# Performance work log

Measured on AMD Instinct MI355X. Metric: run time of the kernel, lower is better.

The kernel has to match this reference:

```python
import jax, jax.numpy as jnp
import numpy as np

HEAD_SIZE = 8
QK_DIM = 512
V_DIM = 512
N = 4096
ATT_DIM = QK_DIM // HEAD_SIZE  # 64
SCALE = ATT_DIM ** (-0.5)
NEG_FILL = jnp.float32(-9e15)


def setup_inputs() -> dict:
    key = jax.random.key(0)
    k1, k2, k3, k4 = jax.random.split(key, 4)
    x1 = jax.random.normal(k1, (N, QK_DIM), dtype=jnp.float32)
    x2 = jax.random.normal(k2, (N, QK_DIM), dtype=jnp.float32)
    v = jax.random.normal(k3, (N, V_DIM), dtype=jnp.float32)
    adj = jax.random.randint(k4, (N, N), 0, 2, dtype=jnp.int32)
    return {"x1": x1, "x2": x2, "v": v, "adj": adj}


def reference(x1, x2, v, adj):
    n = x1.shape[0]
    # [N, H, d] -> [H, N, d]
    q = x1.reshape(n, HEAD_SIZE, -1).transpose(1, 0, 2) * SCALE
    k = x2.reshape(n, HEAD_SIZE, -1).transpose(1, 0, 2)
    vv = v.reshape(n, HEAD_SIZE, -1).transpose(1, 0, 2)
    # [H, N, N] dense scores, masked by adjacency (broadcast over heads)
    scores = jnp.einsum('hnd,hmd->hnm', q, k)
    scores = jnp.where(adj > 0, scores, NEG_FILL)
    attn = jax.nn.softmax(scores, axis=-1)
    out = jnp.einsum('hnm,hmd->hnd', attn, vv)
    # [H, N, d] -> [N, H*d]
    return out.transpose(1, 0, 2).reshape(n, -1)
```

## Files before the change

### kernel.cpp

```cpp
#include <hip/hip_runtime.h>

#define NN 4096
#define HEADS 8
#define DD 64
#define QKD 512

typedef __attribute__((ext_vector_type(8))) short short8;
typedef __attribute__((ext_vector_type(4))) float f32x4;
typedef __attribute__((ext_vector_type(4))) float float4v;
typedef __attribute__((ext_vector_type(4))) int int4v;
typedef unsigned int u32;
typedef unsigned short u16;
typedef unsigned long long u64;

union U8 { u16 u[8]; short8 s; };
union U4 { u32 u[4]; short8 s; };

__device__ __forceinline__ u16 f2bf(float f) {
  u32 u = __float_as_uint(f);
  u += 0x7fffu + ((u >> 16) & 1u);
  return (u16)(u >> 16);
}

__device__ __forceinline__ u32 cvtpk(float lo, float hi) {
  u32 d;
  asm("v_cvt_pk_bf16_f32 %0, %1, %2" : "=v"(d) : "v"(lo), "v"(hi));
  return d;
}

#define GLL(src, dst) __builtin_amdgcn_global_load_lds( \
    (const __attribute__((address_space(1))) void*)(src), \
    (__attribute__((address_space(3))) void*)(dst), 16, 0, 0)

__global__ __launch_bounds__(256) void prepass_fused(
    const float* __restrict__ x2, const float* __restrict__ v,
    const int* __restrict__ adj,
    u16* __restrict__ Kbt, u16* __restrict__ Vbt, u64* __restrict__ Abg)
{
  __shared__ u16 Vtmp[64][80];
  const int b = blockIdx.x;
  const int t = threadIdx.x;

  if (b < 4096) {
    const int row = b;
    const int* src = adj + (size_t)row * NN;
    int4v a0 = *(const int4v*)(src + t * 16);
    int4v a1 = *(const int4v*)(src + t * 16 + 4);
    int4v a2 = *(const int4v*)(src + t * 16 + 8);
    int4v a3 = *(const int4v*)(src + t * 16 + 12);
    u32 bits =
        (u32)(a0.x > 0)         | ((u32)(a0.y > 0) << 1)  |
        ((u32)(a0.z > 0) << 2)  | ((u32)(a0.w > 0) << 3)  |
        ((u32)(a1.x > 0) << 4)  | ((u32)(a1.y > 0) << 5)  |
        ((u32)(a1.z > 0) << 6)  | ((u32)(a1.w > 0) << 7)  |
        ((u32)(a2.x > 0) << 8)  | ((u32)(a2.y > 0) << 9)  |
        ((u32)(a2.z > 0) << 10) | ((u32)(a2.w > 0) << 11) |
        ((u32)(a3.x > 0) << 12) | ((u32)(a3.y > 0) << 13) |
        ((u32)(a3.z > 0) << 14) | ((u32)(a3.w > 0) << 15);
    unsigned char* AB = (unsigned char*)Vtmp;
    *(u16*)(AB + t * 2) = (u16)bits;
    __syncthreads();
    if (t < 64) {
      u64 m = *(const u64*)(AB + t * 8);
      Abg[(size_t)row * 64 + t] = m;
    }
  } else if (b < 4608) {
    const int j = b - 4096;
    const int h = j >> 6, kb = j & 63;
    u16* dst = Kbt + (size_t)j * 4096;
    #pragma unroll
    for (int i = 0; i < 2; i++) {
      int c = t + i * 256;
      int off = c * 16;
      int kr = off >> 7;
      int db = (off & 127) ^ ((kr & 7) << 4);
      int d0 = db >> 1;
      const float* p = x2 + (size_t)(kb * 64 + kr) * QKD + h * DD + d0;
      float4v a0 = *(const float4v*)p;
      float4v a1 = *(const float4v*)(p + 4);
      U8 r;
      r.u[0] = f2bf(a0.x); r.u[1] = f2bf(a0.y); r.u[2] = f2bf(a0.z); r.u[3] = f2bf(a0.w);
      r.u[4] = f2bf(a1.x); r.u[5] = f2bf(a1.y); r.u[6] = f2bf(a1.z); r.u[7] = f2bf(a1.w);
      *(short8*)((char*)dst + off) = r.s;
    }
  } else {
    const int bb = b - 4608;
    const int h = bb >> 6, kb = bb & 63;
    {
      int k = t >> 2, j0 = (t & 3) * 16;
      const float* p = v + (size_t)(kb * 64 + k) * QKD + h * DD + j0;
      float4v a0 = *(const float4v*)p;
      float4v a1 = *(const float4v*)(p + 4);
      float4v a2 = *(const float4v*)(p + 8);
      float4v a3 = *(const float4v*)(p + 12);
      U8 r0, r1;
      r0.u[0] = f2bf(a0.x); r0.u[1] = f2bf(a0.y); r0.u[2] = f2bf(a0.z); r0.u[3] = f2bf(a0.w);
      r0.u[4] = f2bf(a1.x); r0.u[5] = f2bf(a1.y); r0.u[6] = f2bf(a1.z); r0.u[7] = f2bf(a1.w);
      r1.u[0] = f2bf(a2.x); r1.u[1] = f2bf(a2.y); r1.u[2] = f2bf(a2.z); r1.u[3] = f2bf(a2.w);
      r1.u[4] = f2bf(a3.x); r1.u[5] = f2bf(a3.y); r1.u[6] = f2bf(a3.z); r1.u[7] = f2bf(a3.w);
      *(short8*)(&Vtmp[k][j0]) = r0.s;
      *(short8*)(&Vtmp[k][j0 + 8]) = r1.s;
    }
    __syncthreads();
    u16* dst = Vbt + (size_t)bb * 4096;
    #pragma unroll
    for (int i = 0; i < 2; i++) {
      int c = t + i * 256;
      int off = c * 16;
      int vd = off >> 7;
      int kbyte = (off & 127) ^ ((vd & 7) << 4);
      int k0 = kbyte >> 1;
      U8 r;
      #pragma unroll
      for (int jj = 0; jj < 8; jj++) r.u[jj] = Vtmp[k0 + jj][vd];
      *(short8*)((char*)dst + off) = r.s;
    }
  }
}

__global__ __launch_bounds__(256) void attn_fast(
    const float* __restrict__ x1,
    const u64* __restrict__ Abg,
    const u16* __restrict__ Kbt, const u16* __restrict__ Vbt,
    float* __restrict__ out)
{
  __shared__ u16 Klds[2][4096];
  __shared__ u16 Vlds[2][4096];

  const int b = blockIdx.x;
  const int widx = ((b & 7) << 6) | (b >> 3);
  const int qt = widx >> 3;
  const int h = widx & 7;
  const int t = threadIdx.x;
  const int w = t >> 6;
  const int lane = t & 63;
  const int g = lane >> 4;
  const int qi = lane & 15;
  const int qrow = qt * 64 + w * 16 + qi;

  const u16* Ktiles = Kbt + (size_t)h * 64 * 4096;
  const u16* Vtiles = Vbt + (size_t)h * 64 * 4096;
  const u64* arow = Abg + (size_t)qrow * 64;

  const float SCL = 0.125f * 1.4426950408889634f;
  short8 qfrag[2];
  #pragma unroll
  for (int dc = 0; dc < 2; dc++) {
    const float* p = x1 + (size_t)qrow * QKD + h * DD + dc * 32 + g * 8;
    float4v a = *(const float4v*)p;
    float4v c = *(const float4v*)(p + 4);
    U8 r;
    r.u[0] = f2bf(a.x * SCL); r.u[1] = f2bf(a.y * SCL);
    r.u[2] = f2bf(a.z * SCL); r.u[3] = f2bf(a.w * SCL);
    r.u[4] = f2bf(c.x * SCL); r.u[5] = f2bf(c.y * SCL);
    r.u[6] = f2bf(c.z * SCL); r.u[7] = f2bf(c.w * SCL);
    qfrag[dc] = r.s;
  }

  const f32x4 zero = {0.f, 0.f, 0.f, 0.f};
  f32x4 Ot[4] = {zero, zero, zero, zero};
  float mrun = -1e30f;
  float lsum = 0.f;

  {
    const u16* sk = Ktiles + t * 8;
    const u16* sv = Vtiles + t * 8;
    u16* dk = &Klds[0][t * 8];
    u16* dv = &Vlds[0][t * 8];
    GLL(sk, dk);
    GLL(sk + 2048, dk + 2048);
    GLL(sv, dv);
    GLL(sv + 2048, dv + 2048);
  }
  u64 adjcur = arow[0];
  __syncthreads();

  int cur = 0;
  for (int kb = 0; kb < NN / 64; kb++) {
    u64 adjnext = 0;
    if (kb < NN / 64 - 1) {
      const u16* sk = Ktiles + (size_t)(kb + 1) * 4096 + t * 8;
      const u16* sv = Vtiles + (size_t)(kb + 1) * 4096 + t * 8;
      u16* dk = &Klds[cur ^ 1][t * 8];
      u16* dv = &Vlds[cur ^ 1][t * 8];
      GLL(sk, dk);
      GLL(sk + 2048, dk + 2048);
      GLL(sv, dv);
      GLL(sv + 2048, dv + 2048);
      adjnext = arow[kb + 1];
    }

    const char* kbase = (const char*)Klds[cur];
    f32x4 st[4] = {zero, zero, zero, zero};
    __builtin_amdgcn_s_setprio(1);
    #pragma unroll
    for (int tk = 0; tk < 4; tk++) {
      int krow = tk * 16 + qi;
      #pragma unroll
      for (int dc = 0; dc < 2; dc++) {
        int off = (krow * 128 + (dc * 32 + g * 8) * 2) ^ ((krow & 7) << 4);
        short8 af = *(const short8*)(kbase + off);
        st[tk] = __builtin_amdgcn_mfma_f32_16x16x32_bf16(af, qfrag[dc], st[tk], 0, 0, 0);
      }
    }
    __builtin_amdgcn_s_setprio(0);

    u32 blo = (u32)adjcur, bhi = (u32)(adjcur >> 32);

    #pragma unroll
    for (int tk = 0; tk < 4; tk++) {
      u32 half = (tk < 2) ? blo : bhi;
      int bb0 = (tk & 1) * 16 + g * 4;
      #pragma unroll
      for (int r = 0; r < 4; r++) {
        float s = st[tk][r];
        st[tk][r] = ((half >> (bb0 + r)) & 1u) ? s : -9e15f;
      }
    }
    float t0 = fmaxf(fmaxf(st[0][0], st[0][1]), fmaxf(st[0][2], st[0][3]));
    float t1 = fmaxf(fmaxf(st[1][0], st[1][1]), fmaxf(st[1][2], st[1][3]));
    float t2 = fmaxf(fmaxf(st[2][0], st[2][1]), fmaxf(st[2][2], st[2][3]));
    float t3 = fmaxf(fmaxf(st[3][0], st[3][1]), fmaxf(st[3][2], st[3][3]));
    float tmax = fmaxf(fmaxf(t0, t1), fmaxf(t2, t3));
    tmax = fmaxf(tmax, __shfl_xor(tmax, 16));
    tmax = fmaxf(tmax, __shfl_xor(tmax, 32));

    if (!__all(tmax <= mrun)) {
      const float newm = fmaxf(mrun, tmax);
      const float alpha = __builtin_amdgcn_exp2f(mrun - newm);
      lsum *= alpha;
      #pragma unroll
      for (int tv = 0; tv < 4; tv++) {
        Ot[tv][0] *= alpha; Ot[tv][1] *= alpha; Ot[tv][2] *= alpha; Ot[tv][3] *= alpha;
      }
      mrun = newm;
    }

    float psum = 0.f;
    u32 pk[8];
    #pragma unroll
    for (int tk = 0; tk < 4; tk++) {
      float p0 = __builtin_amdgcn_exp2f(st[tk][0] - mrun);
      float p1 = __builtin_amdgcn_exp2f(st[tk][1] - mrun);
      float p2 = __builtin_amdgcn_exp2f(st[tk][2] - mrun);
      float p3 = __builtin_amdgcn_exp2f(st[tk][3] - mrun);
      psum += (p0 + p1) + (p2 + p3);
      pk[tk * 2 + 0] = cvtpk(p0, p1);
      pk[tk * 2 + 1] = cvtpk(p2, p3);
    }
    psum += __shfl_xor(psum, 16);
    psum += __shfl_xor(psum, 32);
    lsum += psum;

    const char* vbase = (const char*)Vlds[cur];
    const int srcbase = qi + ((g & 1) << 5);
    #pragma unroll
    for (int kc = 0; kc < 2; kc++) {
      U4 pf;
      #pragma unroll
      for (int jp = 0; jp < 4; jp++) {
        int src = srcbase + ((jp >> 1) << 4);
        u32 va1 = (u32)__shfl((int)pk[4 * kc + (jp & 1)], src);
        u32 vb1 = (u32)__shfl((int)pk[4 * kc + 2 + (jp & 1)], src);
        pf.u[jp] = (g < 2) ? va1 : vb1;
      }
      __builtin_amdgcn_s_setprio(1);
      #pragma unroll
      for (int tv = 0; tv < 4; tv++) {
        int vd = tv * 16 + qi;
        int off = (vd * 128 + (kc * 32 + g * 8) * 2) ^ ((vd & 7) << 4);
        short8 vfrag = *(const short8*)(vbase + off);
        Ot[tv] = __builtin_amdgcn_mfma_f32_16x16x32_bf16(vfrag, pf.s, Ot[tv], 0, 0, 0);
      }
      __builtin_amdgcn_s_setprio(0);
    }

    __syncthreads();
    adjcur = adjnext;
    cur ^= 1;
  }

  float inv = 1.0f / lsum;
  #pragma unroll
  for (int tv = 0; tv < 4; tv++) {
    float4v o;
    o.x = Ot[tv][0] * inv; o.y = Ot[tv][1] * inv;
    o.z = Ot[tv][2] * inv; o.w = Ot[tv][3] * inv;
    *(float4v*)(out + (size_t)qrow * QKD + h * DD + tv * 16 + g * 4) = o;
  }
}

__global__ __launch_bounds__(512) void attn_fallback(
    const float* __restrict__ x1, const float* __restrict__ x2f,
    const float* __restrict__ vf, const int* __restrict__ adj,
    float* __restrict__ out)
{
  __shared__ u16 Klds[64 * 128];
  __shared__ u16 Vlds[128 * 64];
  __shared__ u64 Abits[64];

  const int b = blockIdx.x;
  const int qt = (b & 7) | ((b >> 5) << 3);
  const int hg = (b >> 3) & 3;
  const int h0 = hg * 2;
  const int t = threadIdx.x;
  const int w = t >> 6;
  const int lane = t & 63;
  const int qsub = w >> 1;
  const int hh = w & 1;
  const int h = h0 + hh;
  const int g = lane >> 4;
  const int qi = lane & 15;
  const int qbase = qt * 64;
  const int q_local = qsub * 16 + qi;
  const int qrow = qbase + q_local;

  const float SCL = 0.125f * 1.4426950408889634f;
  short8 qfrag[2];
  #pragma unroll
  for (int dc = 0; dc < 2; dc++) {
    const float* p = x1 + (size_t)qrow * QKD + h * DD + dc * 32 + g * 8;
    float4v a = *(const float4v*)p;
    float4v c = *(const float4v*)(p + 4);
    U8 r;
    r.u[0] = f2bf(a.x * SCL); r.u[1] = f2bf(a.y * SCL);
    r.u[2] = f2bf(a.z * SCL); r.u[3] = f2bf(a.w * SCL);
    r.u[4] = f2bf(c.x * SCL); r.u[5] = f2bf(c.y * SCL);
    r.u[6] = f2bf(c.z * SCL); r.u[7] = f2bf(c.w * SCL);
    qfrag[dc] = r.s;
  }

  const f32x4 zero = {0.f, 0.f, 0.f, 0.f};
  f32x4 Ot[4] = {zero, zero, zero, zero};
  float mrun = -1e30f;
  float lsum = 0.f;

  for (int kb = 0; kb < NN / 64; kb++) {
    const int k0 = kb * 64;
    __syncthreads();
    #pragma unroll
    for (int i = 0; i < 2; i++) {
      int s = t + i * 512;
      int row = s >> 4, c0 = (s & 15) * 8;
      int off = (row * 256 + c0 * 2) ^ ((row & 7) << 4);
      const float* p = x2f + (size_t)(k0 + row) * QKD + h0 * DD + c0;
      float4v a = *(const float4v*)p;
      float4v c = *(const float4v*)(p + 4);
      U8 r;
      r.u[0]=f2bf(a.x); r.u[1]=f2bf(a.y); r.u[2]=f2bf(a.z); r.u[3]=f2bf(a.w);
      r.u[4]=f2bf(c.x); r.u[5]=f2bf(c.y); r.u[6]=f2bf(c.z); r.u[7]=f2bf(c.w);
      *(short8*)((char*)Klds + off) = r.s;
    }
    {
      int vdg = t & 15, kp = t >> 4;
      int vd0 = vdg * 8, kk = kp * 2;
      u16 ua[8], ub[8];
      const float* pa = vf + (size_t)(k0 + kk) * QKD + h0 * DD + vd0;
      float4v a0 = *(const float4v*)pa;
      float4v a1 = *(const float4v*)(pa + 4);
      float4v b0 = *(const float4v*)(pa + QKD);
      float4v b1 = *(const float4v*)(pa + QKD + 4);
      ua[0]=f2bf(a0.x); ua[1]=f2bf(a0.y); ua[2]=f2bf(a0.z); ua[3]=f2bf(a0.w);
      ua[4]=f2bf(a1.x); ua[5]=f2bf(a1.y); ua[6]=f2bf(a1.z); ua[7]=f2bf(a1.w);
      ub[0]=f2bf(b0.x); ub[1]=f2bf(b0.y); ub[2]=f2bf(b0.z); ub[3]=f2bf(b0.w);
      ub[4]=f2bf(b1.x); ub[5]=f2bf(b1.y); ub[6]=f2bf(b1.z); ub[7]=f2bf(b1.w);
      #pragma unroll
      for (int j = 0; j < 8; j++) {
        u32 pk2 = (u32)ua[j] | ((u32)ub[j] << 16);
        int vd = vd0 + j;
        int off = (vd * 128 + kk * 2) ^ (((vd & 7) ^ ((vd >> 3) & 7)) << 4);
        *(u32*)((char*)Vlds + off) = pk2;
      }
    }
    {
      int row = t >> 3, c8 = t & 7;
      const int* ap = adj + (size_t)(qbase + row) * NN + k0 + c8 * 8;
      int4v a0 = *(const int4v*)ap;
      int4v a1 = *(const int4v*)(ap + 4);
      u32 byteval = (u32)(a0.x > 0)        | ((u32)(a0.y > 0) << 1) |
                    ((u32)(a0.z > 0) << 2) | ((u32)(a0.w > 0) << 3) |
                    ((u32)(a1.x > 0) << 4) | ((u32)(a1.y > 0) << 5) |
                    ((u32)(a1.z > 0) << 6) | ((u32)(a1.w > 0) << 7);
      ((unsigned char*)Abits)[row * 8 + c8] = (unsigned char)byteval;
    }
    __syncthreads();

    f32x4 st[4] = {zero, zero, zero, zero};
    #pragma unroll
    for (int tk = 0; tk < 4; tk++) {
      #pragma unroll
      for (int dc = 0; dc < 2; dc++) {
        int krow = tk * 16 + qi;
        int c = hh * 64 + dc * 32 + g * 8;
        int off = (krow * 256 + c * 2) ^ ((krow & 7) << 4);
        short8 af = *(const short8*)((char*)Klds + off);
        st[tk] = __builtin_amdgcn_mfma_f32_16x16x32_bf16(af, qfrag[dc], st[tk], 0, 0, 0);
      }
    }

    u64 bbm = Abits[q_local];
    u32 blo = (u32)bbm, bhi = (u32)(bbm >> 32);

    float tmax = -1e30f;
    #pragma unroll
    for (int tk = 0; tk < 4; tk++) {
      u32 half = (tk < 2) ? blo : bhi;
      int bb0 = (tk & 1) * 16 + g * 4;
      #pragma unroll
      for (int r = 0; r < 4; r++) {
        float s = st[tk][r];
        s = ((half >> (bb0 + r)) & 1u) ? s : -9e15f;
        st[tk][r] = s;
        tmax = fmaxf(tmax, s);
      }
    }
    tmax = fmaxf(tmax, __shfl_xor(tmax, 16));
    tmax = fmaxf(tmax, __shfl_xor(tmax, 32));
    float newm = fmaxf(mrun, tmax);
    float alpha = __builtin_amdgcn_exp2f(mrun - newm);
    mrun = newm;

    float psum = 0.f;
    u32 pk[8];
    #pragma unroll
    for (int tk = 0; tk < 4; tk++) {
      float p0 = __builtin_amdgcn_exp2f(st[tk][0] - newm);
      float p1 = __builtin_amdgcn_exp2f(st[tk][1] - newm);
      float p2 = __builtin_amdgcn_exp2f(st[tk][2] - newm);
      float p3 = __builtin_amdgcn_exp2f(st[tk][3] - newm);
      psum += (p0 + p1) + (p2 + p3);
      pk[tk * 2 + 0] = (u32)f2bf(p0) | ((u32)f2bf(p1) << 16);
      pk[tk * 2 + 1] = (u32)f2bf(p2) | ((u32)f2bf(p3) << 16);
    }
    psum += __shfl_xor(psum, 16);
    psum += __shfl_xor(psum, 32);
    lsum = lsum * alpha + psum;
    #pragma unroll
    for (int tv = 0; tv < 4; tv++) {
      Ot[tv][0] *= alpha; Ot[tv][1] *= alpha; Ot[tv][2] *= alpha; Ot[tv][3] *= alpha;
    }

    const int srcbase = qi + ((g & 1) << 5);
    #pragma unroll
    for (int kc = 0; kc < 2; kc++) {
      U4 pf;
      #pragma unroll
      for (int jp = 0; jp < 4; jp++) {
        int src = srcbase + ((jp >> 1) << 4);
        u32 va1 = (u32)__shfl((int)pk[4 * kc + (jp & 1)], src);
        u32 vb1 = (u32)__shfl((int)pk[4 * kc + 2 + (jp & 1)], src);
        pf.u[jp] = (g < 2) ? va1 : vb1;
      }
      #pragma unroll
      for (int tv = 0; tv < 4; tv++) {
        int vd = hh * 64 + tv * 16 + qi;
        int off = (vd * 128 + (kc * 32 + g * 8) * 2) ^ (((vd & 7) ^ ((vd >> 3) & 7)) << 4);
        short8 vfrag = *(const short8*)((char*)Vlds + off);
        Ot[tv] = __builtin_amdgcn_mfma_f32_16x16x32_bf16(vfrag, pf.s, Ot[tv], 0, 0, 0);
      }
    }
  }

  float inv = 1.0f / lsum;
  #pragma unroll
  for (int tv = 0; tv < 4; tv++) {
    float4v o;
    o.x = Ot[tv][0] * inv; o.y = Ot[tv][1] * inv;
    o.z = Ot[tv][2] * inv; o.w = Ot[tv][3] * inv;
    *(float4v*)(out + (size_t)qrow * QKD + h * DD + tv * 16 + g * 4) = o;
  }
}

extern "C" void kernel_launch(void* const* d_in, const int* in_sizes, int n_in,
                              void* d_out, int out_size, void* d_ws, size_t ws_size,
                              hipStream_t stream) {
  const float* x1 = (const float*)d_in[0];
  const float* x2 = (const float*)d_in[1];
  const float* v  = (const float*)d_in[2];
  const int* adj  = (const int*)d_in[3];
  float* out = (float*)d_out;

  const size_t szK = (size_t)512 * 4096 * sizeof(u16);
  const size_t szV = szK;
  const size_t szA = (size_t)NN * 64 * sizeof(u64);
  const size_t need = szK + szV + szA;

  if (ws_size >= need && d_ws != nullptr) {
    u16* Kbt = (u16*)d_ws;
    u16* Vbt = (u16*)((char*)d_ws + szK);
    u64* Abg = (u64*)((char*)d_ws + szK + szV);
    prepass_fused<<<dim3(5120), dim3(256), 0, stream>>>(x2, v, adj, Kbt, Vbt, Abg);
    attn_fast<<<dim3(512), dim3(256), 0, stream>>>(x1, Abg, Kbt, Vbt, out);
  } else {
    attn_fallback<<<dim3(256), dim3(512), 0, stream>>>(x1, x2, v, adj, out);
  }
}
```

Before: 209.5 us.

## Split key range across two wave groups per block with softmax merge

```diff
diff --git a/kernel.cpp b/kernel.cpp
--- a/kernel.cpp
+++ b/kernel.cpp
@@ -118,14 +118,14 @@
   }
 }
 
-__global__ __launch_bounds__(256) void attn_fast(
+__global__ __launch_bounds__(512, 4) void attn_fast(
     const float* __restrict__ x1,
     const u64* __restrict__ Abg,
     const u16* __restrict__ Kbt, const u16* __restrict__ Vbt,
     float* __restrict__ out)
 {
-  __shared__ u16 Klds[2][4096];
-  __shared__ u16 Vlds[2][4096];
+  __shared__ u16 KL[2][2][4096];
+  __shared__ u16 VL[2][2][4096];
 
   const int b = blockIdx.x;
   const int widx = ((b & 7) << 6) | (b >> 3);
@@ -136,7 +136,9 @@
   const int lane = t & 63;
   const int g = lane >> 4;
   const int qi = lane & 15;
-  const int qrow = qt * 64 + w * 16 + qi;
+  const int qh = w & 3;
+  const int kpar = w >> 2;
+  const int qrow = qt * 64 + qh * 16 + qi;
 
   const u16* Ktiles = Kbt + (size_t)h * 64 * 4096;
   const u16* Vtiles = Vbt + (size_t)h * 64 * 4096;
@@ -162,35 +164,27 @@
   float mrun = -1e30f;
   float lsum = 0.f;
 
-  {
-    const u16* sk = Ktiles + t * 8;
-    const u16* sv = Vtiles + t * 8;
-    u16* dk = &Klds[0][t * 8];
-    u16* dv = &Vlds[0][t * 8];
-    GLL(sk, dk);
-    GLL(sk + 2048, dk + 2048);
-    GLL(sv, dv);
-    GLL(sv + 2048, dv + 2048);
-  }
-  u64 adjcur = arow[0];
+  GLL(Ktiles + 0 * 4096 + t * 8, &KL[0][0][t * 8]);
+  GLL(Ktiles + 1 * 4096 + t * 8, &KL[1][0][t * 8]);
+  GLL(Vtiles + 0 * 4096 + t * 8, &VL[0][0][t * 8]);
+  GLL(Vtiles + 1 * 4096 + t * 8, &VL[1][0][t * 8]);
+  u64 adjcur = arow[kpar];
   __syncthreads();
 
   int cur = 0;
-  for (int kb = 0; kb < NN / 64; kb++) {
+  for (int i = 0; i < 32; i++) {
     u64 adjnext = 0;
-    if (kb < NN / 64 - 1) {
-      const u16* sk = Ktiles + (size_t)(kb + 1) * 4096 + t * 8;
-      const u16* sv = Vtiles + (size_t)(kb + 1) * 4096 + t * 8;
-      u16* dk = &Klds[cur ^ 1][t * 8];
-      u16* dv = &Vlds[cur ^ 1][t * 8];
-      GLL(sk, dk);
-      GLL(sk + 2048, dk + 2048);
-      GLL(sv, dv);
-      GLL(sv + 2048, dv + 2048);
-      adjnext = arow[kb + 1];
-    }
-
-    const char* kbase = (const char*)Klds[cur];
+    if (i < 31) {
+      const size_t nt = 2 * (size_t)(i + 1);
+      GLL(Ktiles + nt * 4096 + t * 8,       &KL[0][cur ^ 1][t * 8]);
+      GLL(Ktiles + (nt + 1) * 4096 + t * 8, &KL[1][cur ^ 1][t * 8]);
+      GLL(Vtiles + nt * 4096 + t * 8,       &VL[0][cur ^ 1][t * 8]);
+      GLL(Vtiles + (nt + 1) * 4096 + t * 8, &VL[1][cur ^ 1][t * 8]);
+      adjnext = arow[nt + kpar];
+    }
+
+    const char* kbase = (const char*)KL[kpar][cur];
+    const char* vbase = (const char*)VL[kpar][cur];
     f32x4 st[4] = {zero, zero, zero, zero};
     __builtin_amdgcn_s_setprio(1);
     #pragma unroll
@@ -252,7 +246,6 @@
     psum += __shfl_xor(psum, 32);
     lsum += psum;
 
-    const char* vbase = (const char*)Vlds[cur];
     const int srcbase = qi + ((g & 1) << 5);
     #pragma unroll
     for (int kc = 0; kc < 2; kc++) {
@@ -280,13 +273,36 @@
     cur ^= 1;
   }
 
-  float inv = 1.0f / lsum;
-  #pragma unroll
-  for (int tv = 0; tv < 4; tv++) {
-    float4v o;
-    o.x = Ot[tv][0] * inv; o.y = Ot[tv][1] * inv;
-    o.z = Ot[tv][2] * inv; o.w = Ot[tv][3] * inv;
-    *(float4v*)(out + (size_t)qrow * QKD + h * DD + tv * 16 + g * 4) = o;
+  float* mb = (float*)&KL[0][0][0];
+  const int mbase = (qh * 64 + lane) * 20;
+  if (kpar == 1) {
+    #pragma unroll
+    for (int tv = 0; tv < 4; tv++) {
+      mb[mbase + tv * 4 + 0] = Ot[tv][0];
+      mb[mbase + tv * 4 + 1] = Ot[tv][1];
+      mb[mbase + tv * 4 + 2] = Ot[tv][2];
+      mb[mbase + tv * 4 + 3] = Ot[tv][3];
+    }
+    mb[mbase + 16] = mrun;
+    mb[mbase + 17] = lsum;
+  }
+  __syncthreads();
+  if (kpar == 0) {
+    const float m2 = mb[mbase + 16];
+    const float l2 = mb[mbase + 17];
+    const float M = fmaxf(mrun, m2);
+    const float a1 = __builtin_amdgcn_exp2f(mrun - M);
+    const float a2 = __builtin_amdgcn_exp2f(m2 - M);
+    const float inv = 1.0f / (lsum * a1 + l2 * a2);
+    #pragma unroll
+    for (int tv = 0; tv < 4; tv++) {
+      float4v o;
+      o.x = (Ot[tv][0] * a1 + mb[mbase + tv * 4 + 0] * a2) * inv;
+      o.y = (Ot[tv][1] * a1 + mb[mbase + tv * 4 + 1] * a2) * inv;
+      o.z = (Ot[tv][2] * a1 + mb[mbase + tv * 4 + 2] * a2) * inv;
+      o.w = (Ot[tv][3] * a1 + mb[mbase + tv * 4 + 3] * a2) * inv;
+      *(float4v*)(out + (size_t)qrow * QKD + h * DD + tv * 16 + g * 4) = o;
+    }
   }
 }
 
@@ -490,7 +506,7 @@
     u16* Vbt = (u16*)((char*)d_ws + szK);
     u64* Abg = (u64*)((char*)d_ws + szK + szV);
     prepass_fused<<<dim3(5120), dim3(256), 0, stream>>>(x2, v, adj, Kbt, Vbt, Abg);
-    attn_fast<<<dim3(512), dim3(256), 0, stream>>>(x1, Abg, Kbt, Vbt, out);
+    attn_fast<<<dim3(512), dim3(512), 0, stream>>>(x1, Abg, Kbt, Vbt, out);
   } else {
     attn_fallback<<<dim3(256), dim3(512), 0, stream>>>(x1, x2, v, adj, out);
   }
```

Result: faster. 192.8 us (-8.0%).
